# Performance work log

Hardware: AMD Instinct MI355X
Metric: run time of the kernel (lower is better)

Reference implementation:

```python
import jax, jax.numpy as jnp
import numpy as np

B, L, D_MODEL, D_STATE, D_CONV, EXPAND = 2, 1024, 1024, 16, 4, 2
D_INNER = D_MODEL * EXPAND


def setup_inputs() -> dict:
    key = jax.random.key(0)
    ks = jax.random.split(key, 8)
    s = lambda fan: 1.0 / np.sqrt(fan)
    x = jax.random.normal(ks[0], (B, L, D_MODEL), jnp.float32)
    in_proj_w = jax.random.normal(ks[1], (D_MODEL, 2 * D_INNER), jnp.float32) * s(D_MODEL)
    conv_w = jax.random.normal(ks[2], (D_INNER, 1, D_CONV), jnp.float32) * s(D_CONV)
    conv_b = jax.random.normal(ks[3], (D_INNER,), jnp.float32) * 0.01
    x_proj_w = jax.random.normal(ks[4], (D_INNER, 2 * D_STATE + D_INNER), jnp.float32) * s(D_INNER)
    dt_proj_w = jax.random.normal(ks[5], (D_INNER, D_INNER), jnp.float32) * s(D_INNER)
    dt_proj_b = jax.random.normal(ks[6], (D_INNER,), jnp.float32) * 0.01
    A_log = jnp.log(jnp.tile(jnp.arange(1, D_STATE + 1, dtype=jnp.float32)[None, :], (D_INNER, 1)))
    D = jnp.ones((D_INNER,), jnp.float32)
    out_proj_w = jax.random.normal(ks[7], (D_INNER, D_MODEL), jnp.float32) * s(D_INNER)
    return {"x": x, "in_proj_w": in_proj_w, "conv_w": conv_w, "conv_b": conv_b,
            "x_proj_w": x_proj_w, "dt_proj_w": dt_proj_w, "dt_proj_b": dt_proj_b,
            "A_log": A_log, "D": D, "out_proj_w": out_proj_w}


def _mamba_forward(x, in_proj_w, conv_w, conv_b, x_proj_w, dt_proj_w, dt_proj_b, A_log, D, out_proj_w):
    Bb, Ll, _ = x.shape
    d_inner, _, d_conv = conv_w.shape
    d_state = A_log.shape[1]
    # input projection and gate split
    xz = x @ in_proj_w                       # [B, L, 2*Di]
    x_inner, z = jnp.split(xz, 2, axis=-1)   # each [B, L, Di]
    # causal depthwise conv (left pad k-1, truncate to L == torch pad+slice)
    xc = jnp.transpose(x_inner, (0, 2, 1))   # [B, Di, L]
    xc = jax.lax.conv_general_dilated(
        xc, conv_w, window_strides=(1,), padding=[(d_conv - 1, 0)],
        dimension_numbers=("NCH", "OIH", "NCH"), feature_group_count=d_inner)
    xc = xc + conv_b[None, :, None]
    u = jax.nn.silu(jnp.transpose(xc, (0, 2, 1)))  # [B, L, Di]
    # SSM parameter projections
    ssm = u @ x_proj_w                        # [B, L, 2N+Di]
    B_ssm = ssm[..., :d_state]                # [B, L, N]
    C_ssm = ssm[..., d_state:2 * d_state]     # [B, L, N]
    dt = jax.nn.softplus(ssm[..., 2 * d_state:] @ dt_proj_w + dt_proj_b)  # [B, L, Di]
    A_real = -jnp.exp(A_log)                  # [Di, N]
    # selective scan over sequence (recurrence via lax.scan)
    def step(h, inp):
        dt_t, B_t, u_t = inp                  # [B,Di], [B,N], [B,Di]
        dA = jnp.exp(dt_t[..., None] * A_real)            # [B, Di, N]
        dBu = dt_t[..., None] * B_t[:, None, :] * u_t[..., None]
        h = dA * h + dBu
        return h, h
    h0 = jnp.zeros((Bb, d_inner, d_state), x.dtype)
    xs = (jnp.swapaxes(dt, 0, 1), jnp.swapaxes(B_ssm, 0, 1), jnp.swapaxes(u, 0, 1))
    _, states = jax.lax.scan(step, h0, xs)    # [L, B, Di, N]
    y = jnp.einsum("lbdn,lbn->lbd", states, jnp.swapaxes(C_ssm, 0, 1))
    y = jnp.swapaxes(y, 0, 1) + D * u         # skip connection
    y = y * jax.nn.silu(z)                    # gating
    return y @ out_proj_w                     # [B, L, d_model]


def reference(x, in_proj_w, conv_w, conv_b, x_proj_w, dt_proj_w, dt_proj_b, A_log, D, out_proj_w):
    return _mamba_forward(x, in_proj_w, conv_w, conv_b, x_proj_w, dt_proj_w, dt_proj_b, A_log, D, out_proj_w)
```

## Files before the change

kernel.cpp:

```cpp
#include <hip/hip_runtime.h>
#include <hip/hip_bf16.h>

#define BB 2
#define LL 1024
#define DMODEL 1024
#define DINNER 2048
#define DSTATE 16
#define DCONV 4
#define MM (BB * LL)
#define N_XZ 4096
#define N_SSM 2080
#define N_SSM_PAD 2176
#define CCH 32
#define LCH 32

typedef __hip_bfloat16 bf16;
typedef short bf16x8 __attribute__((ext_vector_type(8)));
typedef float f32x4 __attribute__((ext_vector_type(4)));

__device__ __forceinline__ void load16_lds(const bf16* g, bf16* l) {
    __builtin_amdgcn_global_load_lds(
        (const __attribute__((address_space(1))) void*)g,
        (__attribute__((address_space(3))) void*)l,
        16, 0, 0);
}

template<int SWZ>
__device__ __forceinline__ void remap(int id, int NX, int& bx, int& by) {
    if (SWZ >= 0) {
        int xcd = id & 7, slot = id >> 3;
        bx = (xcd << SWZ) + (slot & ((1 << SWZ) - 1));
        by = slot >> SWZ;
    } else { bx = id % NX; by = id / NX; }
}

__global__ __launch_bounds__(256) void prep_kernel(
    const float* __restrict__ x, bf16* __restrict__ xbf,
    const float* __restrict__ w1, bf16* __restrict__ o1,
    const float* __restrict__ w3, bf16* __restrict__ o3,
    const float* __restrict__ w4, bf16* __restrict__ o4,
    const float* __restrict__ w2, bf16* __restrict__ w2bf,
    bf16* __restrict__ w2bc)
{
    int bid = blockIdx.x;
    if (bid >= 14464) {
        bid -= 14464;
        int i = (bid * 256 + threadIdx.x) * 4;
        float4 v = *(const float4*)(x + i);
        xbf[i + 0] = __float2bfloat16(v.x);
        xbf[i + 1] = __float2bfloat16(v.y);
        xbf[i + 2] = __float2bfloat16(v.z);
        xbf[i + 3] = __float2bfloat16(v.w);
        return;
    }
    if (bid >= 10240 && bid < 14400) {
        bid -= 10240;
        int i = (bid * 256 + threadIdx.x) * 4;
        float4 v = *(const float4*)(w2 + i);
        w2bf[i + 0] = __float2bfloat16(v.x);
        w2bf[i + 1] = __float2bfloat16(v.y);
        w2bf[i + 2] = __float2bfloat16(v.z);
        w2bf[i + 3] = __float2bfloat16(v.w);
        return;
    }
    const float* src; bf16* dst; int K, N, tn, tk, srcld;
    if (bid < 4096)        { src = w1; dst = o1; K = 1024; N = 4096; tn = bid & 127; tk = bid >> 7; srcld = N; }
    else if (bid < 8192)   { bid -= 4096; src = w3; dst = o3; K = 2048; N = 2048; tn = bid & 63; tk = bid >> 6; srcld = N; }
    else if (bid < 10240)  { bid -= 8192; src = w4; dst = o4; K = 2048; N = 1024; tn = bid & 31; tk = bid >> 5; srcld = N; }
    else                   { bid -= 14400; src = w2; dst = w2bc; K = 2048; N = 32; tn = 0; tk = bid; srcld = N_SSM; }
    __shared__ float tile[32][33];
    const int nb = tn * 32, kb = tk * 32;
    const int tx = threadIdx.x & 31, ty = threadIdx.x >> 5;
    #pragma unroll
    for (int i = 0; i < 32; i += 8) {
        int k = kb + ty + i, n = nb + tx;
        tile[ty + i][tx] = (k < K && n < N) ? src[(size_t)k * srcld + n] : 0.f;
    }
    __syncthreads();
    #pragma unroll
    for (int i = 0; i < 32; i += 8) {
        int n = nb + ty + i, k = kb + tx;
        if (n < N && k < K) dst[(size_t)n * K + k] = __float2bfloat16(tile[tx][ty + i]);
    }
}

__device__ __forceinline__ void gemm_body128(
    bf16* AsB, bf16* BsB, int bx, int by,
    const bf16* __restrict__ A, int lda,
    const bf16* __restrict__ Wt, int ldw,
    bf16* __restrict__ Cb, int ldc,
    int N, int K)
{
    const int tid = threadIdx.x;
    const int wave = tid >> 6, lane = tid & 63;
    const int wm = (wave >> 1) * 64, wn = (wave & 1) * 64;
    const int m0 = by * 128, n0 = bx * 128;
    const int lm = lane & 15, kq = lane >> 4;

    const int srow = lane >> 3;
    const int schunk = (lane & 7) ^ srow;
    const bf16* gA = A  + (size_t)(m0 + wave * 32 + srow) * lda + schunk * 8;
    const bf16* gB = Wt + (size_t)(n0 + wave * 32 + srow) * ldw + schunk * 8;

    const int NK = K / 64;
    f32x4 acc[4][4] = {};
    const int fsw = lm & 7;

    auto stage = [&](int buf, int it) {
        const int k0 = it * 64;
        bf16* lA = AsB + buf * (128 * 64) + (wave * 32) * 64;
        bf16* lB = BsB + buf * (128 * 64) + (wave * 32) * 64;
        #pragma unroll
        for (int g = 0; g < 4; ++g) {
            load16_lds(gA + (size_t)(8 * g) * lda + k0, lA + (8 * g) * 64);
            load16_lds(gB + (size_t)(8 * g) * ldw + k0, lB + (8 * g) * 64);
        }
    };
    auto compute = [&](int buf) {
        const bf16* Asb = AsB + buf * (128 * 64);
        const bf16* Bsb = BsB + buf * (128 * 64);
        bf16x8 af[4][2], bfr[4][2];
        #pragma unroll
        for (int i = 0; i < 4; ++i)
            #pragma unroll
            for (int t = 0; t < 2; ++t)
                af[i][t] = *(const bf16x8*)(&Asb[(wm + i * 16 + lm) * 64 + ((t * 4 + kq) ^ fsw) * 8]);
        #pragma unroll
        for (int j = 0; j < 4; ++j)
            #pragma unroll
            for (int t = 0; t < 2; ++t)
                bfr[j][t] = *(const bf16x8*)(&Bsb[(wn + j * 16 + lm) * 64 + ((t * 4 + kq) ^ fsw) * 8]);
        #pragma unroll
        for (int t = 0; t < 2; ++t)
            #pragma unroll
            for (int i = 0; i < 4; ++i)
                #pragma unroll
                for (int j = 0; j < 4; ++j)
                    acc[i][j] = __builtin_amdgcn_mfma_f32_16x16x32_bf16(af[i][t], bfr[j][t], acc[i][j], 0, 0, 0);
    };

    stage(0, 0);
    for (int it = 0; it < NK; it += 2) {
        stage(1, it + 1);
        __builtin_amdgcn_s_waitcnt(0x0F78);
        __builtin_amdgcn_s_barrier();
        compute(0);
        __builtin_amdgcn_s_barrier();
        if (it + 2 < NK) {
            stage(0, it + 2);
            __builtin_amdgcn_s_waitcnt(0x0F78);
        } else {
            __builtin_amdgcn_s_waitcnt(0x0F70);
        }
        __builtin_amdgcn_s_barrier();
        compute(1);
        __builtin_amdgcn_s_barrier();
    }

    #pragma unroll
    for (int i = 0; i < 4; ++i) {
        #pragma unroll
        for (int j = 0; j < 4; ++j) {
            int gcol = n0 + wn + j * 16 + lm;
            if (gcol >= N) continue;
            #pragma unroll
            for (int r = 0; r < 4; ++r) {
                int grow = m0 + wm + i * 16 + kq * 4 + r;
                Cb[(size_t)grow * ldc + gcol] = __float2bfloat16(acc[i][j][r]);
            }
        }
    }
}

__global__ __launch_bounds__(256, 2) void mfma_dual128(
    int nblk0, int NX0,
    const bf16* __restrict__ A0, int lda0, const bf16* __restrict__ Wt0, int ldw0,
    bf16* __restrict__ Cb0, int ldc0, int N0, int K0,
    int NX1,
    const bf16* __restrict__ A1, int lda1, const bf16* __restrict__ Wt1, int ldw1,
    bf16* __restrict__ Cb1, int ldc1, int N1, int K1)
{
    __shared__ __align__(16) bf16 As[2 * 128 * 64];
    __shared__ __align__(16) bf16 Bs[2 * 128 * 64];
    int id = blockIdx.x;
    if (id < nblk0) {
        int bx, by; remap<1>(id, NX0, bx, by);
        gemm_body128(As, Bs, bx, by, A0, lda0, Wt0, ldw0, Cb0, ldc0, N0, K0);
    } else {
        int bx, by; remap<2>(id - nblk0, NX1, bx, by);
        gemm_body128(As, Bs, bx, by, A1, lda1, Wt1, ldw1, Cb1, ldc1, N1, K1);
    }
}

template<int EPI>
__device__ __forceinline__ void gemm_body64(
    bf16* AsB, bf16* BsB, int bx, int by,
    const bf16* __restrict__ A, int lda,
    const bf16* __restrict__ Wt, int ldw,
    float* __restrict__ Cf, bf16* __restrict__ Cb, int ldc,
    const float* __restrict__ bias,
    int N, int K, int kbeg, int Kc, bool at)
{
    const int tid = threadIdx.x;
    const int wave = tid >> 6, lane = tid & 63;
    const int wm = (wave >> 1) * 64, wn = (wave & 1) * 32;
    const int m0 = by * 128, n0 = bx * 64;
    const int lm = lane & 15, kq = lane >> 4;

    const int srow = lane >> 3;
    const int schunk = (lane & 7) ^ srow;
    const bf16* gA = A + (size_t)(m0 + wave * 32 + srow) * lda + schunk * 8;
    const bf16* gB = Wt + (size_t)(n0 + wave * 16 + srow) * ldw + schunk * 8;

    const int NK = Kc / 64;
    f32x4 acc[4][2] = {};
    const int fsw = (lm & 7);

    auto stage = [&](int buf, int it) {
        const int k0 = kbeg + it * 64;
        bf16* lA = AsB + buf * (128 * 64) + (wave * 32) * 64;
        bf16* lB = BsB + buf * (64 * 64) + (wave * 16) * 64;
        #pragma unroll
        for (int g = 0; g < 4; ++g)
            load16_lds(gA + (size_t)(8 * g) * lda + k0, lA + (8 * g) * 64);
        #pragma unroll
        for (int g = 0; g < 2; ++g)
            load16_lds(gB + (size_t)(8 * g) * ldw + k0, lB + (8 * g) * 64);
    };
    auto compute = [&](int buf) {
        const bf16* Asb = AsB + buf * (128 * 64);
        const bf16* Bsb = BsB + buf * (64 * 64);
        bf16x8 af[4][2], bfr[2][2];
        #pragma unroll
        for (int i = 0; i < 4; ++i)
            #pragma unroll
            for (int t = 0; t < 2; ++t)
                af[i][t] = *(const bf16x8*)(&Asb[(wm + i * 16 + lm) * 64 + ((t * 4 + kq) ^ fsw) * 8]);
        #pragma unroll
        for (int j = 0; j < 2; ++j)
            #pragma unroll
            for (int t = 0; t < 2; ++t)
                bfr[j][t] = *(const bf16x8*)(&Bsb[(wn + j * 16 + lm) * 64 + ((t * 4 + kq) ^ fsw) * 8]);
        #pragma unroll
        for (int t = 0; t < 2; ++t)
            #pragma unroll
            for (int i = 0; i < 4; ++i)
                #pragma unroll
                for (int j = 0; j < 2; ++j)
                    acc[i][j] = __builtin_amdgcn_mfma_f32_16x16x32_bf16(af[i][t], bfr[j][t], acc[i][j], 0, 0, 0);
    };

    stage(0, 0);
    for (int it = 0; it < NK; it += 2) {
        stage(1, it + 1);
        __builtin_amdgcn_s_waitcnt(0x0F76);
        __builtin_amdgcn_s_barrier();
        compute(0);
        __builtin_amdgcn_s_barrier();
        if (it + 2 < NK) {
            stage(0, it + 2);
            __builtin_amdgcn_s_waitcnt(0x0F76);
        } else {
            __builtin_amdgcn_s_waitcnt(0x0F70);
        }
        __builtin_amdgcn_s_barrier();
        compute(1);
        __builtin_amdgcn_s_barrier();
    }

    #pragma unroll
    for (int i = 0; i < 4; ++i) {
        #pragma unroll
        for (int j = 0; j < 2; ++j) {
            int gcol = n0 + wn + j * 16 + lm;
            if ((EPI == 0 || EPI == 3) && gcol >= N) continue;
            #pragma unroll
            for (int r = 0; r < 4; ++r) {
                int grow = m0 + wm + i * 16 + kq * 4 + r;
                float v = acc[i][j][r];
                if (EPI == 1) {
                    v += bias[gcol];
                    v = (v > 20.f) ? v : log1pf(__expf(v));
                    Cf[(size_t)grow * ldc + gcol] = v;
                } else if (EPI == 2) {
                    if (at) atomicAdd(&Cf[(size_t)grow * ldc + gcol], v);
                    else    Cf[(size_t)grow * ldc + gcol] = v;
                } else if (EPI == 3) {
                    Cf[(size_t)grow * 32 + gcol] = v;
                } else {
                    Cb[(size_t)grow * ldc + gcol] = __float2bfloat16(v);
                }
            }
        }
    }
}

template<int EPI, int KSPLIT = 1, int SWZ = -1>
__global__ __launch_bounds__(256) void mfma_gemm64(
    const bf16* __restrict__ A, int lda,
    const bf16* __restrict__ Wt, int ldw,
    float* __restrict__ Cf, bf16* __restrict__ Cb, int ldc,
    const float* __restrict__ bias,
    int N, int K)
{
    __shared__ __align__(16) bf16 As[2 * 128 * 64];
    __shared__ __align__(16) bf16 Bs[2 * 64 * 64];
    int bx, by;
    if (SWZ >= 0) {
        int id = blockIdx.x + (int)(gridDim.x * blockIdx.y);
        remap<SWZ>(id, gridDim.x, bx, by);
    } else { bx = blockIdx.x; by = blockIdx.y; }
    const int Kc = K / KSPLIT;
    const int kbeg = (KSPLIT > 1) ? blockIdx.z * Kc : 0;
    gemm_body64<EPI>(As, Bs, bx, by, A, lda, Wt, ldw, Cf, Cb, ldc,
                     bias, N, K, kbeg, Kc, KSPLIT > 1);
}

template<int EPI0, int SWZ0, int EPI1, int SWZ1>
__global__ __launch_bounds__(256) void mfma_dual64(
    int nblk0, int NX0,
    const bf16* __restrict__ A0, int lda0, const bf16* __restrict__ Wt0, int ldw0,
    float* __restrict__ Cf0, bf16* __restrict__ Cb0, int ldc0,
    const float* __restrict__ bias0, int N0, int K0,
    int NX1,
    const bf16* __restrict__ A1, int lda1, const bf16* __restrict__ Wt1, int ldw1,
    float* __restrict__ Cf1, bf16* __restrict__ Cb1, int ldc1,
    const float* __restrict__ bias1, int N1, int K1)
{
    __shared__ __align__(16) bf16 As[2 * 128 * 64];
    __shared__ __align__(16) bf16 Bs[2 * 64 * 64];
    int id = blockIdx.x;
    if (id < nblk0) {
        int bx, by; remap<SWZ0>(id, NX0, bx, by);
        gemm_body64<EPI0>(As, Bs, bx, by, A0, lda0, Wt0, ldw0,
                          Cf0, Cb0, ldc0, bias0, N0, K0, 0, K0, false);
    } else {
        id -= nblk0;
        int bx, by; remap<SWZ1>(id, NX1, bx, by);
        gemm_body64<EPI1>(As, Bs, bx, by, A1, lda1, Wt1, ldw1,
                          Cf1, Cb1, ldc1, bias1, N1, K1, 0, K1, false);
    }
}

__global__ void conv_silu_kernel(const bf16* __restrict__ xz,
                                 const float* __restrict__ conv_w,
                                 const float* __restrict__ conv_b,
                                 bf16* __restrict__ u)
{
    int idx = blockIdx.x * blockDim.x + threadIdx.x;
    int d8 = idx & (DINNER / 8 - 1);
    int l  = (idx >> 8) & (LL - 1);
    int b  = idx >> 18;
    int d0 = d8 * 8;

    float acc[8];
    {
        float4 b0 = *(const float4*)(conv_b + d0);
        float4 b1 = *(const float4*)(conv_b + d0 + 4);
        acc[0] = b0.x; acc[1] = b0.y; acc[2] = b0.z; acc[3] = b0.w;
        acc[4] = b1.x; acc[5] = b1.y; acc[6] = b1.z; acc[7] = b1.w;
    }
    #pragma unroll
    for (int j = 0; j < DCONV; ++j) {
        int ll = l - (DCONV - 1) + j;
        if (ll >= 0) {
            bf16x8 v = *(const bf16x8*)(xz + ((size_t)(b * LL + ll)) * N_XZ + d0);
            #pragma unroll
            for (int r = 0; r < 8; ++r) {
                float xv = __uint_as_float(((unsigned)(unsigned short)v[r]) << 16);
                acc[r] = fmaf(conv_w[(d0 + r) * DCONV + j], xv, acc[r]);
            }
        }
    }
    bf16x8 out;
    #pragma unroll
    for (int r = 0; r < 8; ++r) {
        float y = acc[r] / (1.f + __expf(-acc[r]));
        bf16 h = __float2bfloat16(y);
        out[r] = *reinterpret_cast<short*>(&h);
    }
    *(bf16x8*)(u + ((size_t)(b * LL + l)) * DINNER + d0) = out;
}

__global__ __launch_bounds__(256) void scan_phase_a(
    const float* __restrict__ dt, const bf16* __restrict__ u,
    const float* __restrict__ BC,
    const float* __restrict__ A_log,
    float* __restrict__ chunkP, float* __restrict__ chunkH)
{
    const int d = blockIdx.x * 256 + threadIdx.x;
    const int c = blockIdx.y, b = blockIdx.z;
    const int l0 = c * LCH;

    float A[DSTATE];
    {
        const f32x4* ap = (const f32x4*)(A_log + d * DSTATE);
        #pragma unroll
        for (int q = 0; q < 4; ++q) {
            f32x4 v = ap[q];
            #pragma unroll
            for (int r = 0; r < 4; ++r) A[q * 4 + r] = -__expf(v[r]);
        }
    }
    float h[DSTATE];
    #pragma unroll
    for (int n = 0; n < DSTATE; ++n) h[n] = 0.f;
    float sdt = 0.f;

    const float* dtp = dt + ((size_t)b * LL + l0) * DINNER + d;
    const bf16* up = u + ((size_t)b * LL + l0) * DINNER + d;
    const float* bcp = BC + ((size_t)b * LL + l0) * 32;

    #pragma unroll 2
    for (int i = 0; i < LCH; ++i) {
        float dtv = *dtp;
        float uv  = (float)*up;
        float du  = dtv * uv;
        f32x4 Bv[4];
        #pragma unroll
        for (int q = 0; q < 4; ++q) Bv[q] = *(const f32x4*)(bcp + q * 4);
        #pragma unroll
        for (int n = 0; n < DSTATE; ++n) {
            float a = __expf(dtv * A[n]);
            h[n] = fmaf(a, h[n], du * Bv[n >> 2][n & 3]);
        }
        sdt += dtv;
        dtp += DINNER; up += DINNER; bcp += 32;
    }

    size_t idx = (((size_t)b * CCH + c) * DINNER + d) * DSTATE;
    #pragma unroll
    for (int q = 0; q < 4; ++q) {
        f32x4 pv, hv;
        #pragma unroll
        for (int r = 0; r < 4; ++r) { pv[r] = __expf(A[q * 4 + r] * sdt); hv[r] = h[q * 4 + r]; }
        *(f32x4*)(chunkP + idx + q * 4) = pv;
        *(f32x4*)(chunkH + idx + q * 4) = hv;
    }
}

__global__ __launch_bounds__(256) void scan_phase_p(
    const float* __restrict__ chunkP, float* __restrict__ chunkH)
{
    int gid = blockIdx.x * 256 + threadIdx.x;
    int n = gid & 15;
    int d = (gid >> 4) & (DINNER - 1);
    int b = gid >> 15;
    const size_t stride = (size_t)DINNER * DSTATE;
    size_t idx = ((size_t)b * CCH * DINNER + d) * DSTATE + n;
    float H = 0.f;
    for (int c = 0; c < CCH; ++c) {
        float P  = chunkP[idx];
        float hl = chunkH[idx];
        chunkH[idx] = H;
        H = fmaf(P, H, hl);
        idx += stride;
    }
}

__global__ __launch_bounds__(256) void scan_phase_b(
    const float* __restrict__ dt, bf16* __restrict__ u,
    const float* __restrict__ BC, const bf16* __restrict__ xz,
    const float* __restrict__ A_log, const float* __restrict__ Dp,
    const float* __restrict__ chunkH)
{
    const int d = blockIdx.x * 256 + threadIdx.x;
    const int c = blockIdx.y, b = blockIdx.z;
    const int l0 = c * LCH;

    float A[DSTATE];
    {
        const f32x4* ap = (const f32x4*)(A_log + d * DSTATE);
        #pragma unroll
        for (int q = 0; q < 4; ++q) {
            f32x4 v = ap[q];
            #pragma unroll
            for (int r = 0; r < 4; ++r) A[q * 4 + r] = -__expf(v[r]);
        }
    }
    const float Dd = Dp[d];
    float h[DSTATE];
    {
        size_t idx = (((size_t)b * CCH + c) * DINNER + d) * DSTATE;
        #pragma unroll
        for (int q = 0; q < 4; ++q) {
            f32x4 v = *(const f32x4*)(chunkH + idx + q * 4);
            #pragma unroll
            for (int r = 0; r < 4; ++r) h[q * 4 + r] = v[r];
        }
    }

    const float* dtp = dt + ((size_t)b * LL + l0) * DINNER + d;
    bf16* up = u + ((size_t)b * LL + l0) * DINNER + d;
    const float* bcp = BC + ((size_t)b * LL + l0) * 32;
    const bf16* zp = xz + ((size_t)b * LL + l0) * N_XZ + DINNER + d;

    #pragma unroll 2
    for (int i = 0; i < LCH; ++i) {
        float dtv = *dtp;
        float uv  = (float)*up;
        float du  = dtv * uv;
        f32x4 Bv[4], Cv[4];
        #pragma unroll
        for (int q = 0; q < 4; ++q) {
            Bv[q] = *(const f32x4*)(bcp + q * 4);
            Cv[q] = *(const f32x4*)(bcp + 16 + q * 4);
        }
        float acc = 0.f;
        #pragma unroll
        for (int n = 0; n < DSTATE; ++n) {
            float a = __expf(dtv * A[n]);
            h[n] = fmaf(a, h[n], du * Bv[n >> 2][n & 3]);
            acc = fmaf(h[n], Cv[n >> 2][n & 3], acc);
        }
        float zv = (float)*zp;
        acc = fmaf(Dd, uv, acc);
        acc *= zv / (1.f + __expf(-zv));
        *up = __float2bfloat16(acc);
        dtp += DINNER; up += DINNER; bcp += 32; zp += N_XZ;
    }
}

extern "C" void kernel_launch(void* const* d_in, const int* in_sizes, int n_in,
                              void* d_out, int out_size, void* d_ws, size_t ws_size,
                              hipStream_t stream) {
    const float* x         = (const float*)d_in[0];
    const float* in_proj_w = (const float*)d_in[1];
    const float* conv_w    = (const float*)d_in[2];
    const float* conv_b    = (const float*)d_in[3];
    const float* x_proj_w  = (const float*)d_in[4];
    const float* dt_proj_w = (const float*)d_in[5];
    const float* dt_proj_b = (const float*)d_in[6];
    const float* A_log     = (const float*)d_in[7];
    const float* Dp        = (const float*)d_in[8];
    const float* out_proj_w= (const float*)d_in[9];
    float* out = (float*)d_out;

    char* p = (char*)d_ws;
    float* dt   = (float*)p;                          p += (size_t)MM * DINNER * 4;
    bf16*  xbf  = (bf16*)dt;
    bf16*  xz   = (bf16*)p;                           p += (size_t)MM * N_XZ * 2;
    bf16*  u    = (bf16*)p;                           p += (size_t)MM * DINNER * 2;
    bf16*  wft  = (bf16*)p;                           p += (size_t)MM * N_SSM * 2;
    bf16*  Wt1  = (bf16*)p;                           p += (size_t)N_XZ * DMODEL * 2;
    bf16*  w2slot = (bf16*)p;                         p += (size_t)N_SSM_PAD * DINNER * 2;
    bf16*  W2bf = w2slot;
    bf16*  w2bc = w2slot + (size_t)DINNER * N_SSM;
    bf16*  Wt3  = (bf16*)p;                           p += (size_t)DINNER * DINNER * 2;
    bf16*  Wt4  = (bf16*)p;                           p += (size_t)DMODEL * DINNER * 2;
    float* BC   = (float*)p;                          p += (size_t)MM * 32 * 4;
    float* chunkP = (float*)Wt1;
    float* chunkH = (float*)w2slot;

    prep_kernel<<<16512, 256, 0, stream>>>(x, xbf, in_proj_w, Wt1, dt_proj_w, Wt3,
                                           out_proj_w, Wt4, x_proj_w, W2bf, w2bc);
    mfma_dual128<<<768, 256, 0, stream>>>(
        256, 16, Wt3, DINNER, W2bf + 32, N_SSM, wft, DINNER, DINNER, DINNER,
        32, xbf, DMODEL, Wt1, DMODEL, xz, N_XZ, N_XZ, DMODEL);
    {
        int n = BB * LL * DINNER / 8;
        conv_silu_kernel<<<(n + 255) / 256, 256, 0, stream>>>(xz, conv_w, conv_b, u);
    }
    mfma_dual64<1, 2, 3, -1><<<528, 256, 0, stream>>>(
        512, 32, u, DINNER, wft, DINNER, dt, nullptr, DINNER, dt_proj_b, DINNER, DINNER,
        1, u, DINNER, w2bc, DINNER, BC, nullptr, 32, nullptr, 32, DINNER);
    scan_phase_a<<<dim3(DINNER / 256, CCH, BB), 256, 0, stream>>>(dt, u, BC, A_log, chunkP, chunkH);
    scan_phase_p<<<dim3(BB * DINNER * DSTATE / 256), 256, 0, stream>>>(chunkP, chunkH);
    scan_phase_b<<<dim3(DINNER / 256, CCH, BB), 256, 0, stream>>>(dt, u, BC, xz, A_log, Dp, chunkH);
    hipMemsetAsync(out, 0, (size_t)out_size * sizeof(float), stream);
    mfma_gemm64<2, 4, 1><<<dim3(16, 16, 4), 256, 0, stream>>>(
        u, DINNER, Wt4, DINNER, out, nullptr, DMODEL, nullptr, DMODEL, DINNER);
}
```

Before: 336.5 us.

## Split-K the dt and BC projections with atomics and move softplus into scan

The dual GEMM that produces dt and B/C now uses a K-split of 2 for both sub-problems, accumulating with atomic adds. The launch grows from 528 to 1056 blocks so the machine is better filled. Because partial sums can no longer apply a nonlinearity, the dt bias add and softplus move into both scan phases, and the zero-fills of dt, BC and the output are folded into existing kernels, replacing a separate memset. The cost is atomic traffic plus recomputing softplus twice per element in the scans.

```diff
diff --git a/kernel.cpp b/kernel.cpp
--- a/kernel.cpp
+++ b/kernel.cpp
@@ -40,9 +40,22 @@
     const float* __restrict__ w3, bf16* __restrict__ o3,
     const float* __restrict__ w4, bf16* __restrict__ o4,
     const float* __restrict__ w2, bf16* __restrict__ w2bf,
-    bf16* __restrict__ w2bc)
+    bf16* __restrict__ w2bc,
+    float* __restrict__ outz, float* __restrict__ bcz)
 {
     int bid = blockIdx.x;
+    if (bid >= 18560) {
+        int i = ((bid - 18560) * 256 + threadIdx.x) * 4;
+        f32x4 z = {};
+        *(f32x4*)(bcz + i) = z;
+        return;
+    }
+    if (bid >= 16512) {
+        int i = ((bid - 16512) * 256 + threadIdx.x) * 4;
+        f32x4 z = {};
+        *(f32x4*)(outz + i) = z;
+        return;
+    }
     if (bid >= 14464) {
         bid -= 14464;
         int i = (bid * 256 + threadIdx.x) * 4;
@@ -273,7 +286,7 @@
         #pragma unroll
         for (int j = 0; j < 2; ++j) {
             int gcol = n0 + wn + j * 16 + lm;
-            if ((EPI == 0 || EPI == 3) && gcol >= N) continue;
+            if ((EPI == 0 || EPI == 3 || EPI == 4) && gcol >= N) continue;
             #pragma unroll
             for (int r = 0; r < 4; ++r) {
                 int grow = m0 + wm + i * 16 + kq * 4 + r;
@@ -287,6 +300,8 @@
                     else    Cf[(size_t)grow * ldc + gcol] = v;
                 } else if (EPI == 3) {
                     Cf[(size_t)grow * 32 + gcol] = v;
+                } else if (EPI == 4) {
+                    atomicAdd(&Cf[(size_t)grow * 32 + gcol], v);
                 } else {
                     Cb[(size_t)grow * ldc + gcol] = __float2bfloat16(v);
                 }
@@ -316,7 +331,7 @@
                      bias, N, K, kbeg, Kc, KSPLIT > 1);
 }
 
-template<int EPI0, int SWZ0, int EPI1, int SWZ1>
+template<int EPI0, int KS0, int SWZ0, int EPI1, int KS1, int SWZ1>
 __global__ __launch_bounds__(256) void mfma_dual64(
     int nblk0, int NX0,
     const bf16* __restrict__ A0, int lda0, const bf16* __restrict__ Wt0, int ldw0,
@@ -331,23 +346,37 @@
     __shared__ __align__(16) bf16 Bs[2 * 64 * 64];
     int id = blockIdx.x;
     if (id < nblk0) {
-        int bx, by; remap<SWZ0>(id, NX0, bx, by);
+        int kz = (KS0 > 1) ? id % KS0 : 0;
+        int tl = (KS0 > 1) ? id / KS0 : id;
+        int bx, by; remap<SWZ0>(tl, NX0, bx, by);
+        const int Kc = K0 / KS0;
         gemm_body64<EPI0>(As, Bs, bx, by, A0, lda0, Wt0, ldw0,
-                          Cf0, Cb0, ldc0, bias0, N0, K0, 0, K0, false);
+                          Cf0, Cb0, ldc0, bias0, N0, K0, kz * Kc, Kc, KS0 > 1);
     } else {
         id -= nblk0;
-        int bx, by; remap<SWZ1>(id, NX1, bx, by);
+        int kz = (KS1 > 1) ? id % KS1 : 0;
+        int tl = (KS1 > 1) ? id / KS1 : id;
+        int bx, by; remap<SWZ1>(tl, NX1, bx, by);
+        const int Kc = K1 / KS1;
         gemm_body64<EPI1>(As, Bs, bx, by, A1, lda1, Wt1, ldw1,
-                          Cf1, Cb1, ldc1, bias1, N1, K1, 0, K1, false);
+                          Cf1, Cb1, ldc1, bias1, N1, K1, kz * Kc, Kc, KS1 > 1);
     }
 }
 
 __global__ void conv_silu_kernel(const bf16* __restrict__ xz,
                                  const float* __restrict__ conv_w,
                                  const float* __restrict__ conv_b,
-                                 bf16* __restrict__ u)
-{
-    int idx = blockIdx.x * blockDim.x + threadIdx.x;
+                                 bf16* __restrict__ u,
+                                 float* __restrict__ dtz)
+{
+    int bid = blockIdx.x;
+    if (bid < 4096) {
+        int i = (bid * 256 + threadIdx.x) * 4;
+        f32x4 z = {};
+        *(f32x4*)(dtz + i) = z;
+        return;
+    }
+    int idx = (bid - 4096) * 256 + threadIdx.x;
     int d8 = idx & (DINNER / 8 - 1);
     int l  = (idx >> 8) & (LL - 1);
     int b  = idx >> 18;
@@ -384,8 +413,8 @@
 
 __global__ __launch_bounds__(256) void scan_phase_a(
     const float* __restrict__ dt, const bf16* __restrict__ u,
-    const float* __restrict__ BC,
-    const float* __restrict__ A_log,
+    const float* __restrict__ BC, const float* __restrict__ A_log,
+    const float* __restrict__ dtb,
     float* __restrict__ chunkP, float* __restrict__ chunkH)
 {
     const int d = blockIdx.x * 256 + threadIdx.x;
@@ -402,6 +431,7 @@
             for (int r = 0; r < 4; ++r) A[q * 4 + r] = -__expf(v[r]);
         }
     }
+    const float bd = dtb[d];
     float h[DSTATE];
     #pragma unroll
     for (int n = 0; n < DSTATE; ++n) h[n] = 0.f;
@@ -413,7 +443,8 @@
 
     #pragma unroll 2
     for (int i = 0; i < LCH; ++i) {
-        float dtv = *dtp;
+        float dtv = *dtp + bd;
+        dtv = (dtv > 20.f) ? dtv : log1pf(__expf(dtv));
         float uv  = (float)*up;
         float du  = dtv * uv;
         f32x4 Bv[4];
@@ -462,6 +493,7 @@
     const float* __restrict__ dt, bf16* __restrict__ u,
     const float* __restrict__ BC, const bf16* __restrict__ xz,
     const float* __restrict__ A_log, const float* __restrict__ Dp,
+    const float* __restrict__ dtb,
     const float* __restrict__ chunkH)
 {
     const int d = blockIdx.x * 256 + threadIdx.x;
@@ -479,6 +511,7 @@
         }
     }
     const float Dd = Dp[d];
+    const float bd = dtb[d];
     float h[DSTATE];
     {
         size_t idx = (((size_t)b * CCH + c) * DINNER + d) * DSTATE;
@@ -497,7 +530,8 @@
 
     #pragma unroll 2
     for (int i = 0; i < LCH; ++i) {
-        float dtv = *dtp;
+        float dtv = *dtp + bd;
+        dtv = (dtv > 20.f) ? dtv : log1pf(__expf(dtv));
         float uv  = (float)*up;
         float du  = dtv * uv;
         f32x4 Bv[4], Cv[4];
@@ -552,22 +586,22 @@
     float* chunkP = (float*)Wt1;
     float* chunkH = (float*)w2slot;
 
-    prep_kernel<<<16512, 256, 0, stream>>>(x, xbf, in_proj_w, Wt1, dt_proj_w, Wt3,
-                                           out_proj_w, Wt4, x_proj_w, W2bf, w2bc);
+    prep_kernel<<<18624, 256, 0, stream>>>(x, xbf, in_proj_w, Wt1, dt_proj_w, Wt3,
+                                           out_proj_w, Wt4, x_proj_w, W2bf, w2bc,
+                                           out, BC);
     mfma_dual128<<<768, 256, 0, stream>>>(
         256, 16, Wt3, DINNER, W2bf + 32, N_SSM, wft, DINNER, DINNER, DINNER,
         32, xbf, DMODEL, Wt1, DMODEL, xz, N_XZ, N_XZ, DMODEL);
     {
         int n = BB * LL * DINNER / 8;
-        conv_silu_kernel<<<(n + 255) / 256, 256, 0, stream>>>(xz, conv_w, conv_b, u);
-    }
-    mfma_dual64<1, 2, 3, -1><<<528, 256, 0, stream>>>(
-        512, 32, u, DINNER, wft, DINNER, dt, nullptr, DINNER, dt_proj_b, DINNER, DINNER,
+        conv_silu_kernel<<<4096 + (n + 255) / 256, 256, 0, stream>>>(xz, conv_w, conv_b, u, dt);
+    }
+    mfma_dual64<2, 2, 2, 4, 2, -1><<<1056, 256, 0, stream>>>(
+        1024, 32, u, DINNER, wft, DINNER, dt, nullptr, DINNER, nullptr, DINNER, DINNER,
         1, u, DINNER, w2bc, DINNER, BC, nullptr, 32, nullptr, 32, DINNER);
-    scan_phase_a<<<dim3(DINNER / 256, CCH, BB), 256, 0, stream>>>(dt, u, BC, A_log, chunkP, chunkH);
+    scan_phase_a<<<dim3(DINNER / 256, CCH, BB), 256, 0, stream>>>(dt, u, BC, A_log, dt_proj_b, chunkP, chunkH);
     scan_phase_p<<<dim3(BB * DINNER * DSTATE / 256), 256, 0, stream>>>(chunkP, chunkH);
-    scan_phase_b<<<dim3(DINNER / 256, CCH, BB), 256, 0, stream>>>(dt, u, BC, xz, A_log, Dp, chunkH);
-    hipMemsetAsync(out, 0, (size_t)out_size * sizeof(float), stream);
+    scan_phase_b<<<dim3(DINNER / 256, CCH, BB), 256, 0, stream>>>(dt, u, BC, xz, A_log, Dp, dt_proj_b, chunkH);
     mfma_gemm64<2, 4, 1><<<dim3(16, 16, 4), 256, 0, stream>>>(
         u, DINNER, Wt4, DINNER, out, nullptr, DMODEL, nullptr, DMODEL, DINNER);
 }
```

Measured after the change: 363.7 us. +8.1%, slower.
